# Kernel tuning notes

Measured on AMD Instinct MI355X. Metric: run time of the kernel, lower is better.

The kernel has to match this reference:

```python
import jax, jax.numpy as jnp
import numpy as np

EPS = 1e-12  # torch F.normalize eps

def setup_inputs() -> dict:
    key = jax.random.key(0)
    ks = jax.random.split(key, 3)
    B, N, C, H, K = 4, 4096, 512, 8, 64
    x = jax.random.normal(ks[0], (B, N, C), dtype=jnp.float32)
    W_qkvv = jax.random.normal(ks[1], (4 * C, C), dtype=jnp.float32) * (1.0 / np.sqrt(C))
    # init_: uniform(-1/sqrt(K), 1/sqrt(K)) over [N, K]
    std = 1.0 / np.sqrt(K)
    EF = jax.random.uniform(ks[2], (N, K), dtype=jnp.float32, minval=-std, maxval=std)
    temperature = jnp.ones((H, 1, 1), dtype=jnp.float32)
    temperature2 = jnp.ones((H, 1, 1), dtype=jnp.float32)
    return {"x": x, "W_qkvv": W_qkvv, "EF": EF,
            "temperature": temperature, "temperature2": temperature2}

def _l2norm(t):
    # torch.nn.functional.normalize(dim=-1): x / max(||x||_2, eps)
    n = jnp.sqrt(jnp.sum(t * t, axis=-1, keepdims=True))
    return t / jnp.maximum(n, EPS)

def reference(x, W_qkvv, EF, temperature, temperature2):
    B, N, C = x.shape
    H = temperature.shape[0]
    d = C // H
    # fused QKVV projection (no bias)
    qkvv = (x @ W_qkvv.T).reshape(B, N, 4, H, d)
    qkvv = jnp.transpose(qkvv, (2, 0, 3, 1, 4))  # [4,B,H,N,d]
    # transpose last two dims -> [B,H,d,N]
    q = jnp.swapaxes(qkvv[0], -2, -1)
    k = jnp.swapaxes(qkvv[1], -2, -1)
    v_CA = jnp.swapaxes(qkvv[2], -2, -1)
    v_SA = jnp.swapaxes(qkvv[3], -2, -1)
    # Linformer-style EF projection over token axis: [B,H,d,N] x [N,K] -> [B,H,d,K]
    k_proj = jnp.einsum('bhdn,nk->bhdk', k, EF)
    v_proj = jnp.einsum('bhdn,nk->bhdk', v_SA, EF)
    # L2-normalize q,k over token axis
    qn = _l2norm(q)
    kn = _l2norm(k)
    # channel attention: [B,H,d,d]
    attn_CA = jax.nn.softmax(jnp.einsum('bhdn,bhen->bhde', qn, kn) * temperature, axis=-1)
    x_CA = jnp.einsum('bhde,bhen->bhdn', attn_CA, v_CA)           # [B,H,d,N]
    x_CA = jnp.transpose(x_CA, (0, 3, 1, 2)).reshape(B, N, C)      # [B,N,C]
    # spatial attention via projected K: [B,H,N,K]
    attn_SA = jax.nn.softmax(jnp.einsum('bhdn,bhdk->bhnk', qn, k_proj) * temperature2, axis=-1)
    x_SA = jnp.einsum('bhnk,bhdk->bhnd', attn_SA, v_proj)          # [B,H,N,d]
    # faithful to the original: permute(0,3,1,2) then reshape(B,N,C)
    x_SA = jnp.transpose(x_SA, (0, 3, 1, 2)).reshape(B, N, C)
    return x_CA + x_SA
```

## Files before the change

### kernel.cpp

```cpp
#include <hip/hip_runtime.h>

typedef unsigned short u16;
typedef unsigned int u32;
typedef __attribute__((ext_vector_type(8))) short s16x8;
typedef __attribute__((ext_vector_type(4))) float f32x4;

#define MFMA16(a,b,c) __builtin_amdgcn_mfma_f32_16x16x32_bf16(a,b,c,0,0,0)

__device__ __forceinline__ u16 f2bf(float f){
  u32 u = __builtin_bit_cast(u32, f);
  return (u16)((u + 0x7FFFu + ((u >> 16) & 1u)) >> 16);
}
__device__ __forceinline__ float b2f(u16 s){
  u32 u = ((u32)s) << 16;
  return __builtin_bit_cast(float, u);
}
__device__ __forceinline__ void async16(const void* g, void* l){
  __builtin_amdgcn_global_load_lds((const __attribute__((address_space(1))) u32*)g,
                                   (__attribute__((address_space(3))) u32*)l, 16, 0, 0);
}


__global__ __launch_bounds__(256) void k_convert(const float4* __restrict__ x4,
                                                 const float4* __restrict__ w4,
                                                 const float* __restrict__ EF,
                                                 u16* __restrict__ Xb, u16* __restrict__ Wb,
                                                 u16* __restrict__ EFt){
  int i = blockIdx.x * 256 + threadIdx.x;
  if (i < 2097152){
    float4 v = x4[i];
    u32 lo = (u32)f2bf(v.x) | ((u32)f2bf(v.y) << 16);
    u32 hi = (u32)f2bf(v.z) | ((u32)f2bf(v.w) << 16);
    *(uint2*)(&Xb[(size_t)i*4]) = make_uint2(lo, hi);
  } else if (i < 2097152 + 262144){
    int j = i - 2097152;
    float4 v = w4[j];
    u32 lo = (u32)f2bf(v.x) | ((u32)f2bf(v.y) << 16);
    u32 hi = (u32)f2bf(v.z) | ((u32)f2bf(v.w) << 16);
    *(uint2*)(&Wb[(size_t)j*4]) = make_uint2(lo, hi);
  } else if (i < 2097152 + 262144 + 262144){
    int j = i - 2097152 - 262144;
    int kk = j >> 12, nn = j & 4095;
    EFt[(size_t)kk*4096 + nn] = f2bf(EF[(size_t)nn*64 + kk]);
  }
}

__global__ __launch_bounds__(512, 2) void k_gemm(const u16* __restrict__ Wb,
                                                 const u16* __restrict__ Xb,
                                                 u16* __restrict__ Out){
  __shared__ u16 As[2][2][128*64];
  __shared__ u16 Bs[2][2][128*64];
  int bid = blockIdx.x;
  int x = bid & 7, c = bid >> 3;
  int ot = c >> 3, mt = x * 8 + (c & 7);
  int o0 = ot * 256, m0 = mt * 256;
  int t = threadIdx.x;
  int lane = t & 63, wid = t >> 6;
  int wr = wid >> 2, wc = wid & 3;
  int l15 = lane & 15, l4 = lane >> 4;

#define STAGE_TILE(kt_, db_)                                                    \
  {                                                                             \
    int kb_ = (kt_) * 64;                                                       \
    int srow_ = t >> 3, sg_ = (t & 7) ^ (srow_ & 7);                            \
    _Pragma("unroll")                                                           \
    for (int hf = 0; hf < 2; ++hf){                                             \
      _Pragma("unroll")                                                         \
      for (int cc = 0; cc < 2; ++cc){                                           \
        int row = cc*64 + srow_;                                                \
        async16(Wb + (size_t)(o0 + hf*128 + row) * 512 + kb_ + sg_*8,           \
                &As[db_][hf][row*64 + (t & 7)*8]);                              \
        async16(Xb + (size_t)(m0 + hf*128 + row) * 512 + kb_ + sg_*8,           \
                &Bs[db_][hf][row*64 + (t & 7)*8]);                              \
      }                                                                         \
    }                                                                           \
  }

  f32x4 acc[8][4];
#pragma unroll
  for (int a = 0; a < 8; ++a)
#pragma unroll
    for (int b = 0; b < 4; ++b) acc[a][b] = (f32x4){0.f, 0.f, 0.f, 0.f};

  STAGE_TILE(0, 0);
  asm volatile("s_waitcnt vmcnt(0)" ::: "memory");
  __builtin_amdgcn_s_barrier();
  asm volatile("" ::: "memory");

  s16x8 bfr[4];
  for (int kt = 0; kt < 8; ++kt){
    int db = kt & 1;
    const u16* Abase = &As[db][wr][0];
    const u16* Bbase = &Bs[db][wc >> 1][0];
#pragma unroll
    for (int p = 0; p < 4; ++p){
      const int ks = p >> 1, rfh = p & 1;
      s16x8 af[4];
#pragma unroll
      for (int i = 0; i < 4; ++i){
        int row = (rfh*4 + i)*16 + l15;
        af[i] = *(const s16x8*)(Abase + row*64 + ((ks*4 + l4) ^ (row & 7))*8);
      }
      if (rfh == 0){
#pragma unroll
        for (int cf = 0; cf < 4; ++cf){
          int row = (wc & 1)*64 + cf*16 + l15;
          bfr[cf] = *(const s16x8*)(Bbase + row*64 + ((ks*4 + l4) ^ (row & 7))*8);
        }
      }
      if (p == 0 && kt < 7) STAGE_TILE(kt + 1, db ^ 1);
      __builtin_amdgcn_s_barrier();
      asm volatile("" ::: "memory");
      __builtin_amdgcn_s_setprio(1);
#pragma unroll
      for (int i = 0; i < 4; ++i)
#pragma unroll
        for (int cf = 0; cf < 4; ++cf)
          acc[rfh*4 + i][cf] = MFMA16(af[i], bfr[cf], acc[rfh*4 + i][cf]);
      __builtin_amdgcn_s_setprio(0);
      if (p == 3 && kt < 7) asm volatile("s_waitcnt vmcnt(0)" ::: "memory");
      __builtin_amdgcn_s_barrier();
      asm volatile("" ::: "memory");
    }
  }
#undef STAGE_TILE

#pragma unroll
  for (int rf = 0; rf < 8; ++rf)
#pragma unroll
    for (int cf = 0; cf < 4; ++cf){
      int o = o0 + wr*128 + rf*16 + l4*4;
      int m = m0 + wc*64 + cf*16 + l15;
#pragma unroll
      for (int r = 0; r < 4; ++r) Out[(size_t)(o + r) * 16384 + m] = f2bf(acc[rf][cf][r]);
    }
}

__global__ __launch_bounds__(256) void k_rnorm(const u16* __restrict__ QK,
                                               float* __restrict__ rq, float* __restrict__ rk){
  int job = blockIdx.x * 4 + (threadIdx.x >> 6);
  int o = job >> 2, b = job & 3;
  int lane = threadIdx.x & 63;
  const u16* row = QK + (size_t)o * 16384 + (size_t)b * 4096;
  float s = 0.f;
#pragma unroll
  for (int it = 0; it < 8; ++it){
    s16x8 v = *(const s16x8*)(&row[it * 512 + lane * 8]);
#pragma unroll
    for (int j = 0; j < 8; ++j){ float f = b2f((u16)v[j]); s += f * f; }
  }
  for (int off = 32; off; off >>= 1) s += __shfl_down(s, off);
  if (lane == 0){
    float r = 1.f / fmaxf(sqrtf(s), 1e-12f);
    if (o < 512) rq[b * 512 + o] = r;
    else         rk[b * 512 + (o - 512)] = r;
  }
}

__global__ __launch_bounds__(256) void k_acc1(const u16* __restrict__ QK,
                                              const u16* __restrict__ EFt,
                                              float* __restrict__ Pp){
  __shared__ u16 Ab[2][64*128];
  __shared__ u16 Bb[2][64*128];
  int bid = blockIdx.x;
  int p = bid >> 8;
  int rem = bid & 255;
  int bh = rem >> 3, s = rem & 7;
  int b = bh >> 3, h = bh & 7;
  int t = threadIdx.x, lane = t & 63, w = t >> 6, l15 = lane & 15, l4 = lane >> 4;
  int abase = (p == 0 ? 0 : (p == 1 ? 512 : 1536)) + h * 64;
  const u16* Aglob = QK + (size_t)abase * 16384 + (size_t)b * 4096 + s * 512;
  const u16* Bglob;
  size_t bstride;
  if (p == 0){ Bglob = QK + (size_t)(512 + h*64) * 16384 + (size_t)b * 4096 + s * 512; bstride = 16384; }
  else       { Bglob = EFt + s * 512; bstride = 4096; }
  int srow = t >> 4, sslot = t & 15;

#define STAGE_ACC(ch, buf)                                                        \
  {                                                                               \
    int n0_ = (ch) * 128;                                                         \
    _Pragma("unroll")                                                             \
    for (int c = 0; c < 4; ++c){                                                  \
      int row = c*16 + srow;                                                      \
      int sg = sslot ^ (row & 7);                                                 \
      async16(Aglob + (size_t)row * 16384 + n0_ + sg*8, &Ab[buf][row*128 + sslot*8]); \
    }                                                                             \
    _Pragma("unroll")                                                             \
    for (int c = 0; c < 4; ++c){                                                  \
      int row = c*16 + srow;                                                      \
      int sg = sslot ^ (row & 7);                                                 \
      async16(Bglob + (size_t)row * bstride + n0_ + sg*8, &Bb[buf][row*128 + sslot*8]); \
    }                                                                             \
  }

  f32x4 acc[4];
#pragma unroll
  for (int c = 0; c < 4; ++c) acc[c] = (f32x4){0.f,0.f,0.f,0.f};

  STAGE_ACC(0, 0);
#pragma unroll
  for (int ch = 0; ch < 4; ++ch){
    int buf = ch & 1;
    if (ch < 3){
      STAGE_ACC(ch + 1, buf ^ 1);
      asm volatile("s_waitcnt vmcnt(8)" ::: "memory");
    } else {
      asm volatile("s_waitcnt vmcnt(0)" ::: "memory");
    }
    __builtin_amdgcn_s_barrier();
    asm volatile("" ::: "memory");
    int arow = w*16 + l15;
#pragma unroll
    for (int ks = 0; ks < 4; ++ks){
      s16x8 a = *(const s16x8*)(&Ab[buf][arow*128 + (((ks*4 + l4) ^ (arow & 7)))*8]);
#pragma unroll
      for (int cf = 0; cf < 4; ++cf){
        int brow = cf*16 + l15;
        s16x8 bb = *(const s16x8*)(&Bb[buf][brow*128 + (((ks*4 + l4) ^ (brow & 7)))*8]);
        acc[cf] = MFMA16(a, bb, acc[cf]);
      }
    }
    __builtin_amdgcn_s_barrier();
    asm volatile("" ::: "memory");
  }

  float* out = Pp + ((size_t)(bh * 3 + p) * 8 + s) * 4096;
#pragma unroll
  for (int cf = 0; cf < 4; ++cf)
#pragma unroll
    for (int r = 0; r < 4; ++r){
      int rr = w*16 + l4*4 + r;
      int cc = cf*16 + l15;
      int off = (p == 1) ? (cc * 64 + rr) : (rr * 64 + cc);
      out[off] = acc[cf][r];
    }
#undef STAGE_ACC
}

__global__ __launch_bounds__(256) void k_fin(const float* __restrict__ Pp,
                                             const float* __restrict__ rq,
                                             const float* __restrict__ rk,
                                             const float* __restrict__ t1,
                                             const float* __restrict__ t2,
                                             u16* __restrict__ Pca,
                                             u16* __restrict__ kpb,
                                             u16* __restrict__ vpb){
  int bid = blockIdx.x;
  int bh = bid >> 2, rg = bid & 3;
  int b = bh >> 3, h = bh & 7;
  int t = threadIdx.x;
  int lr = t >> 4, c4 = t & 15;
  int row = rg * 16 + lr;
  const float* base = Pp + (size_t)bh * 3 * 8 * 4096 + row*64 + c4*4;
  float t1h = t1[h], t2h = t2[h];
  const float* rqh = rq + b*512 + h*64;
  const float* rkh = rk + b*512 + h*64;
  int so = row*64 + (((c4 >> 1) ^ (row & 7)) << 3) + ((c4 & 1) << 2);

  {
    f32x4 a = (f32x4){0.f,0.f,0.f,0.f};
#pragma unroll
    for (int s = 0; s < 8; ++s) a += *(const f32x4*)(base + (size_t)s * 4096);
    float sq = rqh[row] * t1h;
    float v[4];
#pragma unroll
    for (int j = 0; j < 4; ++j) v[j] = a[j] * sq * rkh[c4*4 + j];
    float mx = fmaxf(fmaxf(v[0], v[1]), fmaxf(v[2], v[3]));
    mx = fmaxf(mx, __shfl_xor(mx, 1));
    mx = fmaxf(mx, __shfl_xor(mx, 2));
    mx = fmaxf(mx, __shfl_xor(mx, 4));
    mx = fmaxf(mx, __shfl_xor(mx, 8));
    float sum = 0.f;
#pragma unroll
    for (int j = 0; j < 4; ++j){ v[j] = __expf(v[j] - mx); sum += v[j]; }
    sum += __shfl_xor(sum, 1);
    sum += __shfl_xor(sum, 2);
    sum += __shfl_xor(sum, 4);
    sum += __shfl_xor(sum, 8);
    float inv = 1.f / sum;
    u32 lo = (u32)f2bf(v[0]*inv) | ((u32)f2bf(v[1]*inv) << 16);
    u32 hi = (u32)f2bf(v[2]*inv) | ((u32)f2bf(v[3]*inv) << 16);
    *(uint2*)(&Pca[(size_t)bh*4096 + so]) = make_uint2(lo, hi);
  }
  {
    const float* p1 = base + 8 * 4096;
    f32x4 a = (f32x4){0.f,0.f,0.f,0.f};
#pragma unroll
    for (int s = 0; s < 8; ++s) a += *(const f32x4*)(p1 + (size_t)s * 4096);
    float v[4];
#pragma unroll
    for (int j = 0; j < 4; ++j) v[j] = a[j] * rqh[c4*4 + j] * t2h;
    u32 lo = (u32)f2bf(v[0]) | ((u32)f2bf(v[1]) << 16);
    u32 hi = (u32)f2bf(v[2]) | ((u32)f2bf(v[3]) << 16);
    *(uint2*)(&kpb[(size_t)bh*4096 + so]) = make_uint2(lo, hi);
  }
  {
    const float* p2 = base + 16 * 4096;
    f32x4 a = (f32x4){0.f,0.f,0.f,0.f};
#pragma unroll
    for (int s = 0; s < 8; ++s) a += *(const f32x4*)(p2 + (size_t)s * 4096);
    u32 lo = (u32)f2bf(a[0]) | ((u32)f2bf(a[1]) << 16);
    u32 hi = (u32)f2bf(a[2]) | ((u32)f2bf(a[3]) << 16);
    *(uint2*)(&vpb[(size_t)bh*4096 + so]) = make_uint2(lo, hi);
  }
}

__global__ __launch_bounds__(256) void k_ca_pv(const u16* __restrict__ QK,
                                               const u16* __restrict__ Pca,
                                               float* __restrict__ out){
  __shared__ u16 Pl[64*64];
  __shared__ u16 Vt[64*64];
  __shared__ float Sx[64*64];
  int bid = blockIdx.x;
  int ch = bid & 63, bh = bid >> 6, b = bh >> 3, h = bh & 7;
  int n0 = ch * 64;
  int t = threadIdx.x, lane = t & 63, w = t >> 6, l15 = lane & 15, l4 = lane >> 4;
  {
    const u16* src = Pca + (size_t)bh * 4096;
#pragma unroll
    for (int c = 0; c < 2; ++c)
      async16(src + (c*256 + t)*8, &Pl[(c*256 + t)*8]);
  }
  const u16* Vg = QK + (size_t)(1024 + h*64) * 16384 + (size_t)b*4096 + n0;
#pragma unroll
  for (int pass = 0; pass < 2; ++pass){
    int idx = pass*256 + t;
    int e = idx >> 3, j0 = (idx & 7) * 8, g = idx & 7;
    s16x8 v = *(const s16x8*)(Vg + (size_t)e * 16384 + j0);
#pragma unroll
    for (int i = 0; i < 8; ++i){
      int jj = (i + e + g) & 7;
      int j = j0 + jj;
      Vt[j*64 + ((((e>>3) ^ jj)) << 3) + (e & 7)] = (u16)v[jj];
    }
  }
  __syncthreads();
  f32x4 acc[4];
#pragma unroll
  for (int c = 0; c < 4; ++c) acc[c] = (f32x4){0.f,0.f,0.f,0.f};
  int ar = w*16 + l15;
#pragma unroll
  for (int ks = 0; ks < 2; ++ks){
    s16x8 a = *(const s16x8*)(&Pl[ar*64 + (((ks*4 + l4) ^ (ar & 7)))*8]);
#pragma unroll
    for (int cf = 0; cf < 4; ++cf){
      int br = cf*16 + l15;
      s16x8 bb = *(const s16x8*)(&Vt[br*64 + (((ks*4 + l4) ^ (br & 7)))*8]);
      acc[cf] = MFMA16(a, bb, acc[cf]);
    }
  }
#pragma unroll
  for (int cf = 0; cf < 4; ++cf)
#pragma unroll
    for (int r = 0; r < 4; ++r){
      int d = w*16 + l4*4 + r, j = cf*16 + l15;
      Sx[j*64 + d] = acc[cf][r];
    }
  __syncthreads();
#pragma unroll
  for (int i = 0; i < 4; ++i){
    int idx = t + 256 * i;
    int j = idx >> 4, v = idx & 15;
    float4 val;
    val.x = Sx[j*64 + v*4 + 0]; val.y = Sx[j*64 + v*4 + 1];
    val.z = Sx[j*64 + v*4 + 2]; val.w = Sx[j*64 + v*4 + 3];
    *(float4*)(&out[((size_t)(b*4096 + n0 + j)) * 512 + h*64 + v*4]) = val;
  }
}

__global__ __launch_bounds__(256) void k_sa(const u16* __restrict__ QK,
                                            const u16* __restrict__ kpb,
                                            const u16* __restrict__ vpb,
                                            float* __restrict__ out){
  __shared__ u16 Qt[64*64];
  __shared__ u16 kpl[64*64];
  __shared__ u16 vpl[64*64];
  __shared__ float Sf[64*64];
  int bid = blockIdx.x;
  int ch = bid & 63, bh = bid >> 6, b = bh >> 3, h = bh & 7;
  int n0 = ch * 64;
  int t = threadIdx.x, lane = t & 63, w = t >> 6, l15 = lane & 15, l4 = lane >> 4;
#pragma unroll
  for (int c = 0; c < 2; ++c){
    async16(kpb + (size_t)bh*4096 + (c*256 + t)*8, &kpl[(c*256 + t)*8]);
    async16(vpb + (size_t)bh*4096 + (c*256 + t)*8, &vpl[(c*256 + t)*8]);
  }
  const u16* Qg = QK + (size_t)(h*64) * 16384 + (size_t)b*4096 + n0;
#pragma unroll
  for (int pass = 0; pass < 2; ++pass){
    int idx = pass*256 + t;
    int dd = idx >> 3, j0 = (idx & 7) * 8, g = idx & 7;
    s16x8 v = *(const s16x8*)(Qg + (size_t)dd * 16384 + j0);
#pragma unroll
    for (int i = 0; i < 8; ++i){
      int jj = (i + dd + g) & 7;
      int j = j0 + jj;
      Qt[j*64 + ((((dd>>3) ^ jj)) << 3) + (dd & 7)] = (u16)v[jj];
    }
  }
  __syncthreads();
  f32x4 acc[4];
#pragma unroll
  for (int c = 0; c < 4; ++c) acc[c] = (f32x4){0.f,0.f,0.f,0.f};
  int ar = w*16 + l15;
#pragma unroll
  for (int ks = 0; ks < 2; ++ks){
    s16x8 a = *(const s16x8*)(&Qt[ar*64 + (((ks*4 + l4) ^ (ar & 7)))*8]);
#pragma unroll
    for (int cf = 0; cf < 4; ++cf){
      int br = cf*16 + l15;
      s16x8 bb = *(const s16x8*)(&kpl[br*64 + (((ks*4 + l4) ^ (br & 7)))*8]);
      acc[cf] = MFMA16(a, bb, acc[cf]);
    }
  }
#pragma unroll
  for (int r = 0; r < 4; ++r){
    float mx = fmaxf(fmaxf(acc[0][r], acc[1][r]), fmaxf(acc[2][r], acc[3][r]));
    mx = fmaxf(mx, __shfl_xor(mx, 1));
    mx = fmaxf(mx, __shfl_xor(mx, 2));
    mx = fmaxf(mx, __shfl_xor(mx, 4));
    mx = fmaxf(mx, __shfl_xor(mx, 8));
    float sum = 0.f;
#pragma unroll
    for (int cf = 0; cf < 4; ++cf){ acc[cf][r] = __expf(acc[cf][r] - mx); sum += acc[cf][r]; }
    sum += __shfl_xor(sum, 1);
    sum += __shfl_xor(sum, 2);
    sum += __shfl_xor(sum, 4);
    sum += __shfl_xor(sum, 8);
    float inv = 1.f / sum;
#pragma unroll
    for (int cf = 0; cf < 4; ++cf) acc[cf][r] *= inv;
  }
#pragma unroll
  for (int cf = 0; cf < 4; ++cf)
#pragma unroll
    for (int r = 0; r < 4; ++r){
      int j = w*16 + l4*4 + r;
      int kslot = cf*2 + (l15 >> 3);
      Qt[j*64 + ((kslot ^ (j & 7)) << 3) + (l15 & 7)] = f2bf(acc[cf][r]);
    }
  __syncthreads();
  f32x4 acc2[4];
#pragma unroll
  for (int c = 0; c < 4; ++c) acc2[c] = (f32x4){0.f,0.f,0.f,0.f};
#pragma unroll
  for (int ks = 0; ks < 2; ++ks){
    s16x8 a = *(const s16x8*)(&Qt[ar*64 + (((ks*4 + l4) ^ (ar & 7)))*8]);
#pragma unroll
    for (int cf = 0; cf < 4; ++cf){
      int br = cf*16 + l15;
      s16x8 bb = *(const s16x8*)(&vpl[br*64 + (((ks*4 + l4) ^ (br & 7)))*8]);
      acc2[cf] = MFMA16(a, bb, acc2[cf]);
    }
  }
#pragma unroll
  for (int cf = 0; cf < 4; ++cf)
#pragma unroll
    for (int r = 0; r < 4; ++r){
      int j = w*16 + l4*4 + r, dd = cf*16 + l15;
      Sf[dd*64 + j] = acc2[cf][r];
    }
  __syncthreads();
#pragma unroll
  for (int i = 0; i < 4; ++i){
    int idx = t + 256 * i;
    int dd = idx >> 4, v = idx & 15;
    size_t p = (size_t)b*2097152 + (size_t)dd*32768 + (size_t)h*4096 + n0 + v*4;
    float4 cur = *(float4*)(&out[p]);
    cur.x += Sf[dd*64 + v*4 + 0]; cur.y += Sf[dd*64 + v*4 + 1];
    cur.z += Sf[dd*64 + v*4 + 2]; cur.w += Sf[dd*64 + v*4 + 3];
    *(float4*)(&out[p]) = cur;
  }
}

extern "C" void kernel_launch(void* const* d_in, const int* in_sizes, int n_in,
                              void* d_out, int out_size, void* d_ws, size_t ws_size,
                              hipStream_t stream) {
  const float* x  = (const float*)d_in[0];
  const float* Wq = (const float*)d_in[1];
  const float* EF = (const float*)d_in[2];
  const float* t1 = (const float*)d_in[3];
  const float* t2 = (const float*)d_in[4];
  float* out = (float*)d_out;

  u16* Xb  = (u16*)d_ws;
  u16* Wb  = Xb + 8388608;
  u16* EFt = Wb + 1048576;
  u16* QK  = EFt + 262144;
  float* rq  = (float*)(QK + 33554432);
  float* rk  = rq + 2048;
  u16* kpb = (u16*)(rk + 2048);
  u16* vpb = kpb + 131072;
  u16* Pca = vpb + 131072;
  float* Pp = (float*)d_ws;

  k_convert<<<10240, 256, 0, stream>>>((const float4*)x, (const float4*)Wq, EF, Xb, Wb, EFt);
  k_gemm   <<<512,  512, 0, stream>>>(Wb, Xb, QK);
  k_rnorm  <<<1024, 256, 0, stream>>>(QK, rq, rk);
  k_acc1   <<<768,  256, 0, stream>>>(QK, EFt, Pp);
  k_fin    <<<128,  256, 0, stream>>>(Pp, rq, rk, t1, t2, Pca, kpb, vpb);
  k_ca_pv  <<<2048, 256, 0, stream>>>(QK, Pca, out);
  k_sa     <<<2048, 256, 0, stream>>>(QK, kpb, vpb, out);
}
```

Baseline: 191.3 us.

## Stage GEMM epilogue through LDS and loop CA/SA kernels over four chunks

The GEMM epilogue now writes bf16 results into a swizzled LDS tile and stores full 16-byte rows to global memory, replacing scattered 2-byte stores. The CA and SA kernels each process four 64-token chunks per block, with 512 blocks instead of 2048. This reuses the P/kp/vp tiles loaded once per block and prefetches the next V/Q chunk into registers while the current one computes. Those kernels also drop the fp32 LDS staging for output and write float4 results straight from MFMA accumulators, at the cost of less coalesced output stores and fewer blocks in flight.

```diff
diff --git a/kernel.cpp b/kernel.cpp
--- a/kernel.cpp
+++ b/kernel.cpp
@@ -125,15 +125,33 @@
   }
 #undef STAGE_TILE
 
-#pragma unroll
-  for (int rf = 0; rf < 8; ++rf)
-#pragma unroll
-    for (int cf = 0; cf < 4; ++cf){
-      int o = o0 + wr*128 + rf*16 + l4*4;
-      int m = m0 + wc*64 + cf*16 + l15;
-#pragma unroll
-      for (int r = 0; r < 4; ++r) Out[(size_t)(o + r) * 16384 + m] = f2bf(acc[rf][cf][r]);
-    }
+  u16* Cl = (u16*)&As[0][0][0];
+  int trow = t >> 2;
+  int tsl = (t & 3) * 8;
+#pragma unroll
+  for (int pass = 0; pass < 2; ++pass){
+    if (pass) __syncthreads();
+#pragma unroll
+    for (int rf = 0; rf < 4; ++rf)
+#pragma unroll
+      for (int cf = 0; cf < 4; ++cf){
+        int col = wc*64 + cf*16 + l15;
+        int cs = col >> 3, ci = col & 7;
+#pragma unroll
+        for (int r = 0; r < 4; ++r){
+          int row = wr*64 + rf*16 + l4*4 + r;
+          Cl[row*256 + ((cs ^ (row & 7)) << 3) + ci] = f2bf(acc[pass*4 + rf][cf][r]);
+        }
+      }
+    __syncthreads();
+    int o = o0 + ((trow >> 6) * 128) + (trow & 63) + pass*64;
+#pragma unroll
+    for (int i = 0; i < 8; ++i){
+      int s = tsl + i;
+      uint4 val = *(const uint4*)(&Cl[trow*256 + ((s ^ (trow & 7)) << 3)]);
+      *(uint4*)(&Out[(size_t)o * 16384 + m0 + s*8]) = val;
+    }
+  }
 }
 
 __global__ __launch_bounds__(256) void k_rnorm(const u16* __restrict__ QK,
@@ -310,10 +328,8 @@
                                                float* __restrict__ out){
   __shared__ u16 Pl[64*64];
   __shared__ u16 Vt[64*64];
-  __shared__ float Sx[64*64];
   int bid = blockIdx.x;
-  int ch = bid & 63, bh = bid >> 6, b = bh >> 3, h = bh & 7;
-  int n0 = ch * 64;
+  int cg = bid & 15, bh = bid >> 4, b = bh >> 3, h = bh & 7;
   int t = threadIdx.x, lane = t & 63, w = t >> 6, l15 = lane & 15, l4 = lane >> 4;
   {
     const u16* src = Pca + (size_t)bh * 4096;
@@ -321,50 +337,49 @@
     for (int c = 0; c < 2; ++c)
       async16(src + (c*256 + t)*8, &Pl[(c*256 + t)*8]);
   }
-  const u16* Vg = QK + (size_t)(1024 + h*64) * 16384 + (size_t)b*4096 + n0;
-#pragma unroll
-  for (int pass = 0; pass < 2; ++pass){
-    int idx = pass*256 + t;
-    int e = idx >> 3, j0 = (idx & 7) * 8, g = idx & 7;
-    s16x8 v = *(const s16x8*)(Vg + (size_t)e * 16384 + j0);
+  const u16* Vg = QK + (size_t)(1024 + h*64) * 16384 + (size_t)b*4096;
+  int e_a = t >> 3, j0 = (t & 7) * 8, g = t & 7;
+  int e_b = e_a + 32;
+  int ar = w*16 + l15;
+  s16x8 va = *(const s16x8*)(Vg + (size_t)e_a * 16384 + cg*256 + j0);
+  s16x8 vb = *(const s16x8*)(Vg + (size_t)e_b * 16384 + cg*256 + j0);
+
+  for (int c = 0; c < 4; ++c){
+    int n0 = cg*256 + c*64;
 #pragma unroll
     for (int i = 0; i < 8; ++i){
-      int jj = (i + e + g) & 7;
-      int j = j0 + jj;
-      Vt[j*64 + ((((e>>3) ^ jj)) << 3) + (e & 7)] = (u16)v[jj];
-    }
-  }
-  __syncthreads();
-  f32x4 acc[4];
-#pragma unroll
-  for (int c = 0; c < 4; ++c) acc[c] = (f32x4){0.f,0.f,0.f,0.f};
-  int ar = w*16 + l15;
-#pragma unroll
-  for (int ks = 0; ks < 2; ++ks){
-    s16x8 a = *(const s16x8*)(&Pl[ar*64 + (((ks*4 + l4) ^ (ar & 7)))*8]);
+      int jj = (i + e_a + g) & 7;
+      Vt[(j0 + jj)*64 + (((e_a>>3) ^ jj) << 3) + (e_a & 7)] = (u16)va[jj];
+    }
+#pragma unroll
+    for (int i = 0; i < 8; ++i){
+      int jj = (i + e_b + g) & 7;
+      Vt[(j0 + jj)*64 + (((e_b>>3) ^ jj) << 3) + (e_b & 7)] = (u16)vb[jj];
+    }
+    __syncthreads();
+    if (c < 3){
+      va = *(const s16x8*)(Vg + (size_t)e_a * 16384 + n0 + 64 + j0);
+      vb = *(const s16x8*)(Vg + (size_t)e_b * 16384 + n0 + 64 + j0);
+    }
+    f32x4 acc[4];
+#pragma unroll
+    for (int q = 0; q < 4; ++q) acc[q] = (f32x4){0.f,0.f,0.f,0.f};
+#pragma unroll
+    for (int ks = 0; ks < 2; ++ks){
+      s16x8 a = *(const s16x8*)(&Pl[ar*64 + (((ks*4 + l4) ^ (ar & 7)))*8]);
+#pragma unroll
+      for (int cf = 0; cf < 4; ++cf){
+        int br = cf*16 + l15;
+        s16x8 bb = *(const s16x8*)(&Vt[br*64 + (((ks*4 + l4) ^ (br & 7)))*8]);
+        acc[cf] = MFMA16(a, bb, acc[cf]);
+      }
+    }
 #pragma unroll
     for (int cf = 0; cf < 4; ++cf){
-      int br = cf*16 + l15;
-      s16x8 bb = *(const s16x8*)(&Vt[br*64 + (((ks*4 + l4) ^ (br & 7)))*8]);
-      acc[cf] = MFMA16(a, bb, acc[cf]);
-    }
-  }
-#pragma unroll
-  for (int cf = 0; cf < 4; ++cf)
-#pragma unroll
-    for (int r = 0; r < 4; ++r){
-      int d = w*16 + l4*4 + r, j = cf*16 + l15;
-      Sx[j*64 + d] = acc[cf][r];
-    }
-  __syncthreads();
-#pragma unroll
-  for (int i = 0; i < 4; ++i){
-    int idx = t + 256 * i;
-    int j = idx >> 4, v = idx & 15;
-    float4 val;
-    val.x = Sx[j*64 + v*4 + 0]; val.y = Sx[j*64 + v*4 + 1];
-    val.z = Sx[j*64 + v*4 + 2]; val.w = Sx[j*64 + v*4 + 3];
-    *(float4*)(&out[((size_t)(b*4096 + n0 + j)) * 512 + h*64 + v*4]) = val;
+      float4 val = make_float4(acc[cf][0], acc[cf][1], acc[cf][2], acc[cf][3]);
+      *(float4*)(&out[((size_t)(b*4096 + n0 + cf*16 + l15))*512 + h*64 + w*16 + l4*4]) = val;
+    }
+    __syncthreads();
   }
 }
 
@@ -375,101 +390,102 @@
   __shared__ u16 Qt[64*64];
   __shared__ u16 kpl[64*64];
   __shared__ u16 vpl[64*64];
-  __shared__ float Sf[64*64];
   int bid = blockIdx.x;
-  int ch = bid & 63, bh = bid >> 6, b = bh >> 3, h = bh & 7;
-  int n0 = ch * 64;
+  int cg = bid & 15, bh = bid >> 4, b = bh >> 3, h = bh & 7;
   int t = threadIdx.x, lane = t & 63, w = t >> 6, l15 = lane & 15, l4 = lane >> 4;
 #pragma unroll
   for (int c = 0; c < 2; ++c){
     async16(kpb + (size_t)bh*4096 + (c*256 + t)*8, &kpl[(c*256 + t)*8]);
     async16(vpb + (size_t)bh*4096 + (c*256 + t)*8, &vpl[(c*256 + t)*8]);
   }
-  const u16* Qg = QK + (size_t)(h*64) * 16384 + (size_t)b*4096 + n0;
-#pragma unroll
-  for (int pass = 0; pass < 2; ++pass){
-    int idx = pass*256 + t;
-    int dd = idx >> 3, j0 = (idx & 7) * 8, g = idx & 7;
-    s16x8 v = *(const s16x8*)(Qg + (size_t)dd * 16384 + j0);
+  const u16* Qg = QK + (size_t)(h*64) * 16384 + (size_t)b*4096;
+  int e_a = t >> 3, j0 = (t & 7) * 8, g = t & 7;
+  int e_b = e_a + 32;
+  int ar = w*16 + l15;
+  s16x8 qa = *(const s16x8*)(Qg + (size_t)e_a * 16384 + cg*256 + j0);
+  s16x8 qb = *(const s16x8*)(Qg + (size_t)e_b * 16384 + cg*256 + j0);
+
+  for (int c = 0; c < 4; ++c){
+    int n0 = cg*256 + c*64;
 #pragma unroll
     for (int i = 0; i < 8; ++i){
-      int jj = (i + dd + g) & 7;
-      int j = j0 + jj;
-      Qt[j*64 + ((((dd>>3) ^ jj)) << 3) + (dd & 7)] = (u16)v[jj];
-    }
-  }
-  __syncthreads();
-  f32x4 acc[4];
-#pragma unroll
-  for (int c = 0; c < 4; ++c) acc[c] = (f32x4){0.f,0.f,0.f,0.f};
-  int ar = w*16 + l15;
-#pragma unroll
-  for (int ks = 0; ks < 2; ++ks){
-    s16x8 a = *(const s16x8*)(&Qt[ar*64 + (((ks*4 + l4) ^ (ar & 7)))*8]);
+      int jj = (i + e_a + g) & 7;
+      Qt[(j0 + jj)*64 + (((e_a>>3) ^ jj) << 3) + (e_a & 7)] = (u16)qa[jj];
+    }
+#pragma unroll
+    for (int i = 0; i < 8; ++i){
+      int jj = (i + e_b + g) & 7;
+      Qt[(j0 + jj)*64 + (((e_b>>3) ^ jj) << 3) + (e_b & 7)] = (u16)qb[jj];
+    }
+    __syncthreads();
+    if (c < 3){
+      qa = *(const s16x8*)(Qg + (size_t)e_a * 16384 + n0 + 64 + j0);
+      qb = *(const s16x8*)(Qg + (size_t)e_b * 16384 + n0 + 64 + j0);
+    }
+    float4 cur[4];
+    size_t pb = (size_t)b*2097152 + (size_t)h*4096 + n0 + w*16 + l4*4;
+#pragma unroll
+    for (int cf = 0; cf < 4; ++cf)
+      cur[cf] = *(const float4*)(&out[pb + (size_t)(cf*16 + l15)*32768]);
+    f32x4 acc[4];
+#pragma unroll
+    for (int q = 0; q < 4; ++q) acc[q] = (f32x4){0.f,0.f,0.f,0.f};
+#pragma unroll
+    for (int ks = 0; ks < 2; ++ks){
+      s16x8 a = *(const s16x8*)(&Qt[ar*64 + (((ks*4 + l4) ^ (ar & 7)))*8]);
+#pragma unroll
+      for (int cf = 0; cf < 4; ++cf){
+        int br = cf*16 + l15;
+        s16x8 bb = *(const s16x8*)(&kpl[br*64 + (((ks*4 + l4) ^ (br & 7)))*8]);
+        acc[cf] = MFMA16(a, bb, acc[cf]);
+      }
+    }
+#pragma unroll
+    for (int r = 0; r < 4; ++r){
+      float mx = fmaxf(fmaxf(acc[0][r], acc[1][r]), fmaxf(acc[2][r], acc[3][r]));
+      mx = fmaxf(mx, __shfl_xor(mx, 1));
+      mx = fmaxf(mx, __shfl_xor(mx, 2));
+      mx = fmaxf(mx, __shfl_xor(mx, 4));
+      mx = fmaxf(mx, __shfl_xor(mx, 8));
+      float sum = 0.f;
+#pragma unroll
+      for (int cf = 0; cf < 4; ++cf){ acc[cf][r] = __expf(acc[cf][r] - mx); sum += acc[cf][r]; }
+      sum += __shfl_xor(sum, 1);
+      sum += __shfl_xor(sum, 2);
+      sum += __shfl_xor(sum, 4);
+      sum += __shfl_xor(sum, 8);
+      float inv = 1.f / sum;
+#pragma unroll
+      for (int cf = 0; cf < 4; ++cf) acc[cf][r] *= inv;
+    }
+#pragma unroll
+    for (int cf = 0; cf < 4; ++cf)
+#pragma unroll
+      for (int r = 0; r < 4; ++r){
+        int j = w*16 + l4*4 + r;
+        int kslot = cf*2 + (l15 >> 3);
+        Qt[j*64 + ((kslot ^ (j & 7)) << 3) + (l15 & 7)] = f2bf(acc[cf][r]);
+      }
+    f32x4 acc2[4];
+#pragma unroll
+    for (int q = 0; q < 4; ++q) acc2[q] = (f32x4){0.f,0.f,0.f,0.f};
+#pragma unroll
+    for (int ks = 0; ks < 2; ++ks){
+      s16x8 a = *(const s16x8*)(&Qt[ar*64 + (((ks*4 + l4) ^ (ar & 7)))*8]);
+#pragma unroll
+      for (int cf = 0; cf < 4; ++cf){
+        int br = cf*16 + l15;
+        s16x8 bb = *(const s16x8*)(&vpl[br*64 + (((ks*4 + l4) ^ (br & 7)))*8]);
+        acc2[cf] = MFMA16(a, bb, acc2[cf]);
+      }
+    }
 #pragma unroll
     for (int cf = 0; cf < 4; ++cf){
-      int br = cf*16 + l15;
-      s16x8 bb = *(const s16x8*)(&kpl[br*64 + (((ks*4 + l4) ^ (br & 7)))*8]);
-      acc[cf] = MFMA16(a, bb, acc[cf]);
-    }
-  }
-#pragma unroll
-  for (int r = 0; r < 4; ++r){
-    float mx = fmaxf(fmaxf(acc[0][r], acc[1][r]), fmaxf(acc[2][r], acc[3][r]));
-    mx = fmaxf(mx, __shfl_xor(mx, 1));
-    mx = fmaxf(mx, __shfl_xor(mx, 2));
-    mx = fmaxf(mx, __shfl_xor(mx, 4));
-    mx = fmaxf(mx, __shfl_xor(mx, 8));
-    float sum = 0.f;
-#pragma unroll
-    for (int cf = 0; cf < 4; ++cf){ acc[cf][r] = __expf(acc[cf][r] - mx); sum += acc[cf][r]; }
-    sum += __shfl_xor(sum, 1);
-    sum += __shfl_xor(sum, 2);
-    sum += __shfl_xor(sum, 4);
-    sum += __shfl_xor(sum, 8);
-    float inv = 1.f / sum;
-#pragma unroll
-    for (int cf = 0; cf < 4; ++cf) acc[cf][r] *= inv;
-  }
-#pragma unroll
-  for (int cf = 0; cf < 4; ++cf)
-#pragma unroll
-    for (int r = 0; r < 4; ++r){
-      int j = w*16 + l4*4 + r;
-      int kslot = cf*2 + (l15 >> 3);
-      Qt[j*64 + ((kslot ^ (j & 7)) << 3) + (l15 & 7)] = f2bf(acc[cf][r]);
-    }
-  __syncthreads();
-  f32x4 acc2[4];
-#pragma unroll
-  for (int c = 0; c < 4; ++c) acc2[c] = (f32x4){0.f,0.f,0.f,0.f};
-#pragma unroll
-  for (int ks = 0; ks < 2; ++ks){
-    s16x8 a = *(const s16x8*)(&Qt[ar*64 + (((ks*4 + l4) ^ (ar & 7)))*8]);
-#pragma unroll
-    for (int cf = 0; cf < 4; ++cf){
-      int br = cf*16 + l15;
-      s16x8 bb = *(const s16x8*)(&vpl[br*64 + (((ks*4 + l4) ^ (br & 7)))*8]);
-      acc2[cf] = MFMA16(a, bb, acc2[cf]);
-    }
-  }
-#pragma unroll
-  for (int cf = 0; cf < 4; ++cf)
-#pragma unroll
-    for (int r = 0; r < 4; ++r){
-      int j = w*16 + l4*4 + r, dd = cf*16 + l15;
-      Sf[dd*64 + j] = acc2[cf][r];
-    }
-  __syncthreads();
-#pragma unroll
-  for (int i = 0; i < 4; ++i){
-    int idx = t + 256 * i;
-    int dd = idx >> 4, v = idx & 15;
-    size_t p = (size_t)b*2097152 + (size_t)dd*32768 + (size_t)h*4096 + n0 + v*4;
-    float4 cur = *(float4*)(&out[p]);
-    cur.x += Sf[dd*64 + v*4 + 0]; cur.y += Sf[dd*64 + v*4 + 1];
-    cur.z += Sf[dd*64 + v*4 + 2]; cur.w += Sf[dd*64 + v*4 + 3];
-    *(float4*)(&out[p]) = cur;
+      float4 v = cur[cf];
+      v.x += acc2[cf][0]; v.y += acc2[cf][1]; v.z += acc2[cf][2]; v.w += acc2[cf][3];
+      *(float4*)(&out[pb + (size_t)(cf*16 + l15)*32768]) = v;
+    }
+    __syncthreads();
   }
 }
 
@@ -499,6 +515,6 @@
   k_rnorm  <<<1024, 256, 0, stream>>>(QK, rq, rk);
   k_acc1   <<<768,  256, 0, stream>>>(QK, EFt, Pp);
   k_fin    <<<128,  256, 0, stream>>>(Pp, rq, rk, t1, t2, Pca, kpb, vpb);
-  k_ca_pv  <<<2048, 256, 0, stream>>>(QK, Pca, out);
-  k_sa     <<<2048, 256, 0, stream>>>(QK, kpb, vpb, out);
-}
+  k_ca_pv  <<<512,  256, 0, stream>>>(QK, Pca, out);
+  k_sa     <<<512,  256, 0, stream>>>(QK, kpb, vpb, out);
+}
```

Result: slower. 204.3 us (+6.8%).
